# Optimization experiments

Hardware: AMD Instinct MI355X
Metric: run time of the kernel (lower is better)

The kernel has to match this reference:

```python
import jax, jax.numpy as jnp
import numpy as np

WINDOW = (1, 7, 7)
DIM_HEAD = 32


def _rel_pos_index(ws):
    d, h, w = ws
    coords = np.stack(np.meshgrid(np.arange(d), np.arange(h), np.arange(w), indexing='ij'))
    cf = coords.reshape(3, -1)                      # [3, N]
    rel = (cf[:, :, None] - cf[:, None, :]).transpose(1, 2, 0).copy()  # [N, N, 3]
    rel[..., 0] += d - 1
    rel[..., 1] += h - 1
    rel[..., 2] += w - 1
    rel[..., 0] *= (2 * h - 1) * (2 * w - 1)
    rel[..., 1] *= (2 * w - 1)
    return jnp.asarray(rel.sum(-1))                 # [N, N] int32, N = 49


REL_IDX = _rel_pos_index(WINDOW)


def setup_inputs() -> dict:
    key = jax.random.key(0)
    k1, k2, k3, k4, k5 = jax.random.split(key, 5)
    B, X, Y, W1, W2, D = 4, 32, 32, 7, 7, 512
    heads = D // DIM_HEAD
    n_bias = (2 * WINDOW[0] - 1) * (2 * WINDOW[1] - 1) * (2 * WINDOW[2] - 1)  # 169
    s = 1.0 / np.sqrt(D)
    return {
        'x': jax.random.normal(k1, (B, X, Y, W1, W2, D), jnp.float32),
        'y': jax.random.normal(k2, (B, X, Y, W1, W2, D), jnp.float32),
        'Wq': jax.random.normal(k3, (D, D), jnp.float32) * s,
        'Wkv': jax.random.normal(k4, (D, 2 * D), jnp.float32) * s,
        'bias_table': jax.random.normal(k5, (n_bias, heads), jnp.float32) * 0.02,
    }


def reference(x, y, Wq, Wkv, bias_table):
    B, X, Y, W1, W2, D = x.shape
    h = D // DIM_HEAD
    n = W1 * W2                                     # 49 tokens per window
    scale = DIM_HEAD ** -0.5

    xr = x.reshape(B * X * Y, n, D)                 # [Bw, n, D]
    yr = y.reshape(B * X * Y, n, D)

    q = xr @ Wq                                     # [Bw, n, D]
    kv = yr @ Wkv                                   # [Bw, n, 2D]
    k, v = kv[..., :D], kv[..., D:]

    def to_heads(t):
        return t.reshape(t.shape[0], n, h, DIM_HEAD).transpose(0, 2, 1, 3)  # [Bw, h, n, dh]

    q, k, v = to_heads(q), to_heads(k), to_heads(v)

    sim = jnp.einsum('bhid,bhjd->bhij', q, k) * scale   # [Bw, h, n, n]
    bias = bias_table[REL_IDX]                          # [n, n, h]
    sim = sim + bias.transpose(2, 0, 1)[None]           # broadcast over windows

    attn = jax.nn.softmax(sim, axis=-1)
    out = jnp.einsum('bhij,bhjd->bhid', attn, v)        # [Bw, h, n, dh]
    out = out.transpose(0, 2, 1, 3).reshape(B * X * Y, W1, W2, D)
    return out.reshape(B, X, Y, W1, W2, D)
```

## Files before the change

kernel.cpp:

```cpp
#include <hip/hip_runtime.h>


typedef __bf16 bf16x8 __attribute__((ext_vector_type(8)));
typedef __attribute__((ext_vector_type(4))) float f32x4;

#define DEVI __device__ __forceinline__

DEVI unsigned short f2bf(float f) {
  union { float f; unsigned u; } v; v.f = f;
  unsigned r = v.u + 0x7FFFu + ((v.u >> 16) & 1u);
  return (unsigned short)(r >> 16);
}

#define MFMA16(a, b, c) __builtin_amdgcn_mfma_f32_16x16x32_bf16((a), (b), (c), 0, 0, 0)

__global__ void prep_kernel(const float* __restrict__ Wq, const float* __restrict__ Wkv,
                            const float* __restrict__ bt, char* __restrict__ ws) {
  int t = blockIdx.x * 256 + threadIdx.x;
  if (t < 786432) {
    int e = t & 7, lane = (t >> 3) & 63, ks = (t >> 9) & 15, nt = (t >> 13) & 1,
        h = (t >> 14) & 15, T = t >> 18;
    int row = ks * 32 + (lane >> 4) * 8 + e;
    int col = h * 32 + nt * 16 + (lane & 15);
    float v;
    if (T == 0)      v = Wq[row * 512 + col] * 0.17677669529663687f;
    else if (T == 1) v = Wkv[row * 1024 + col];
    else             v = Wkv[row * 1024 + 512 + col];
    ((unsigned short*)ws)[t] = f2bf(v);
  }
  if (t < 262144) {
    int r = t & 3, lane = (t >> 2) & 63, nt = (t >> 8) & 3, mt = (t >> 10) & 3,
        h = (t >> 12) & 15;
    int i = mt * 16 + (lane >> 4) * 4 + r;
    int j = nt * 16 + (lane & 15);
    float v;
    if (j >= 49)      v = -1e30f;
    else if (i >= 49) v = 0.0f;
    else {
      int hi = i / 7, wi = i % 7, hj = j / 7, wj = j % 7;
      v = bt[((hi - hj + 6) * 13 + (wi - wj + 6)) * 16 + h];
    }
    ((float*)(ws + 1572864))[t] = v;
  }
}

DEVI bf16x8 ldXY(const char* base, int row, int kc) {
  unsigned a = ((unsigned)(row * 1024 + kc * 2)) ^ (((unsigned)row & 7u) << 4);
  return *(const bf16x8*)(base + a);
}
DEVI bf16x8 ldXY_c(const char* base, int row, int kc) {
  int rc = row < 48 ? row : 48;
  bf16x8 v = ldXY(base, rc, kc);
  if (row > 48) {
    union { long long z[2]; bf16x8 v; } u; u.z[0] = 0; u.z[1] = 0;
    v = u.v;
  }
  return v;
}
DEVI bf16x8 ldQK(const char* base, int row, int kc) {
  int rc = row < 48 ? row : 48;
  unsigned a = ((unsigned)(rc * 64 + kc * 2)) ^ (((unsigned)rc & 3u) << 4);
  return *(const bf16x8*)(base + a);
}
DEVI bf16x8 ldP(const char* base, int row, int kc) {
  int rc = row < 48 ? row : 48;
  unsigned a = ((unsigned)(rc * 128 + kc * 2)) ^ (((unsigned)rc & 7u) << 4);
  return *(const bf16x8*)(base + a);
}
DEVI bf16x8 ldVT(const char* base, int dh, int kc) {
  unsigned a = ((unsigned)(dh * 128 + kc * 2)) ^ (((unsigned)dh & 7u) << 4);
  return *(const bf16x8*)(base + a);
}

__global__ __launch_bounds__(512, 2)
void attn_kernel(const float* __restrict__ x, const float* __restrict__ y,
                 const char* __restrict__ wsW, const float* __restrict__ biasD,
                 float* __restrict__ out) {
  extern __shared__ char smem[];
  char* xb = smem;
  char* yb = smem + 50176;
  const int tid = threadIdx.x;
  const int lane = tid & 63, wave = tid >> 6;
  const int p = wave >> 1, sub = wave & 1;
  const int g = lane >> 4, lr = lane & 15;
  char* wb = smem + 100352 + p * 10624;
  char* qb = wb;
  char* kb = wb + 3136;
  char* vt = wb + 6272;
  char* pb = wb;
  float* sb = (float*)(wb + 10368);

  const int bw = blockIdx.x;
  const float* xs = x + (size_t)bw * 25088;
  const float* ys = y + (size_t)bw * 25088;

  for (int it = tid; it < 6272; it += 512) {
    float4 v = ((const float4*)xs)[it];
    float4 w = ((const float4*)ys)[it];
    int i = it >> 7;
    int k = (it & 127) << 2;
    unsigned a = ((unsigned)(i * 1024 + k * 2)) ^ (((unsigned)i & 7u) << 4);
    uint2 ux, uy;
    ux.x = (unsigned)f2bf(v.x) | ((unsigned)f2bf(v.y) << 16);
    ux.y = (unsigned)f2bf(v.z) | ((unsigned)f2bf(v.w) << 16);
    uy.x = (unsigned)f2bf(w.x) | ((unsigned)f2bf(w.y) << 16);
    uy.y = (unsigned)f2bf(w.z) | ((unsigned)f2bf(w.w) << 16);
    *(uint2*)(xb + a) = ux;
    *(uint2*)(yb + a) = uy;
  }

  const bf16x8* wsQ = (const bf16x8*)wsW;
  const bf16x8* wsK = (const bf16x8*)(wsW + 524288);
  const bf16x8* wsV = (const bf16x8*)(wsW + 1048576);
  const f32x4* bD = (const f32x4*)biasD;
  const f32x4 fz = {0.f, 0.f, 0.f, 0.f};

  for (int hi = 0; hi < 4; ++hi) {
    const int h = p * 4 + hi;

    __syncthreads();

    f32x4 accq[4];
    #pragma unroll
    for (int mt = 0; mt < 4; ++mt) accq[mt] = fz;
    {
      const bf16x8* pQ = wsQ + (size_t)((h * 2 + sub) * 16) * 64 + lane;
      bf16x8 bq[16];
      #pragma unroll
      for (int ks = 0; ks < 16; ++ks) bq[ks] = pQ[ks * 64];
      #pragma unroll
      for (int ks = 0; ks < 16; ++ks) {
        int kc = ks * 32 + g * 8;
        accq[0] = MFMA16(ldXY(xb, lr, kc),        bq[ks], accq[0]);
        accq[1] = MFMA16(ldXY(xb, lr + 16, kc),   bq[ks], accq[1]);
        accq[2] = MFMA16(ldXY(xb, lr + 32, kc),   bq[ks], accq[2]);
        accq[3] = MFMA16(ldXY_c(xb, lr + 48, kc), bq[ks], accq[3]);
      }
    }
    #pragma unroll
    for (int mt = 0; mt < 4; ++mt)
      #pragma unroll
      for (int r = 0; r < 4; ++r) {
        int row = mt * 16 + g * 4 + r;
        if (row < 49) {
          unsigned a = ((unsigned)(row * 64 + (sub * 16 + lr) * 2)) ^ (((unsigned)row & 3u) << 4);
          *(unsigned short*)(qb + a) = f2bf(accq[mt][r]);
        }
      }

    f32x4 acck[4], accv[4];
    #pragma unroll
    for (int mt = 0; mt < 4; ++mt) { acck[mt] = fz; accv[mt] = fz; }
    {
      const bf16x8* pK = wsK + (size_t)((h * 2 + sub) * 16) * 64 + lane;
      const bf16x8* pV = wsV + (size_t)((h * 2 + sub) * 16) * 64 + lane;
      bf16x8 ksr[8], vsr[8];
      #pragma unroll
      for (int i = 0; i < 8; ++i) { ksr[i] = pK[i * 64]; vsr[i] = pV[i * 64]; }
      #pragma unroll
      for (int ks = 0; ks < 16; ++ks) {
        bf16x8 bk = ksr[ks & 7], bv = vsr[ks & 7];
        if (ks < 8) {
          ksr[ks & 7] = pK[(ks + 8) * 64];
          vsr[ks & 7] = pV[(ks + 8) * 64];
        }
        int kc = ks * 32 + g * 8;
        bf16x8 a0 = ldXY(yb, lr, kc);
        bf16x8 a1 = ldXY(yb, lr + 16, kc);
        bf16x8 a2 = ldXY(yb, lr + 32, kc);
        bf16x8 a3 = ldXY_c(yb, lr + 48, kc);
        acck[0] = MFMA16(a0, bk, acck[0]);
        acck[1] = MFMA16(a1, bk, acck[1]);
        acck[2] = MFMA16(a2, bk, acck[2]);
        acck[3] = MFMA16(a3, bk, acck[3]);
        accv[0] = MFMA16(a0, bv, accv[0]);
        accv[1] = MFMA16(a1, bv, accv[1]);
        accv[2] = MFMA16(a2, bv, accv[2]);
        accv[3] = MFMA16(a3, bv, accv[3]);
      }
    }
    #pragma unroll
    for (int mt = 0; mt < 4; ++mt) {
      #pragma unroll
      for (int r = 0; r < 4; ++r) {
        int row = mt * 16 + g * 4 + r;
        if (row < 49) {
          unsigned a = ((unsigned)(row * 64 + (sub * 16 + lr) * 2)) ^ (((unsigned)row & 3u) << 4);
          *(unsigned short*)(kb + a) = f2bf(acck[mt][r]);
        }
      }
      int dh = sub * 16 + lr;
      int t0 = mt * 16 + g * 4;
      unsigned av = ((unsigned)(dh * 128 + t0 * 2)) ^ (((unsigned)dh & 7u) << 4);
      uint2 pk;
      pk.x = (unsigned)f2bf(accv[mt][0]) | ((unsigned)f2bf(accv[mt][1]) << 16);
      pk.y = (unsigned)f2bf(accv[mt][2]) | ((unsigned)f2bf(accv[mt][3]) << 16);
      *(uint2*)(vt + av) = pk;
    }

    __syncthreads();

    f32x4 bias[2][4];
    #pragma unroll
    for (int mi = 0; mi < 2; ++mi)
      #pragma unroll
      for (int nt = 0; nt < 4; ++nt)
        bias[mi][nt] = bD[(size_t)(((h * 4 + sub * 2 + mi) * 4 + nt) * 64 + lane)];

    bf16x8 qa[2], kf[4];
    #pragma unroll
    for (int mi = 0; mi < 2; ++mi) qa[mi] = ldQK(qb, sub * 32 + mi * 16 + lr, g * 8);
    #pragma unroll
    for (int nt = 0; nt < 4; ++nt) kf[nt] = ldQK(kb, nt * 16 + lr, g * 8);
    f32x4 accs[2][4];
    #pragma unroll
    for (int mi = 0; mi < 2; ++mi)
      #pragma unroll
      for (int nt = 0; nt < 4; ++nt)
        accs[mi][nt] = MFMA16(qa[mi], kf[nt], fz);

    float sinv[2][4];
    #pragma unroll
    for (int mi = 0; mi < 2; ++mi) {
      f32x4 vals[4];
      #pragma unroll
      for (int nt = 0; nt < 4; ++nt)
        vals[nt] = accs[mi][nt] + bias[mi][nt];
      #pragma unroll
      for (int r = 0; r < 4; ++r) {
        float m = fmaxf(fmaxf(vals[0][r], vals[1][r]), fmaxf(vals[2][r], vals[3][r]));
        m = fmaxf(m, __shfl_xor(m, 1));
        m = fmaxf(m, __shfl_xor(m, 2));
        m = fmaxf(m, __shfl_xor(m, 4));
        m = fmaxf(m, __shfl_xor(m, 8));
        float s = 0.f;
        #pragma unroll
        for (int nt = 0; nt < 4; ++nt) {
          float pv = __expf(vals[nt][r] - m);
          vals[nt][r] = pv;
          s += pv;
        }
        s += __shfl_xor(s, 1);
        s += __shfl_xor(s, 2);
        s += __shfl_xor(s, 4);
        s += __shfl_xor(s, 8);
        sinv[mi][r] = 1.0f / s;
      }
      accs[mi][0] = vals[0]; accs[mi][1] = vals[1];
      accs[mi][2] = vals[2]; accs[mi][3] = vals[3];
    }

    __syncthreads();

    #pragma unroll
    for (int mi = 0; mi < 2; ++mi) {
      int mt_g = sub * 2 + mi;
      #pragma unroll
      for (int r = 0; r < 4; ++r) {
        int row = mt_g * 16 + g * 4 + r;
        if (row < 49) {
          #pragma unroll
          for (int nt = 0; nt < 4; ++nt) {
            unsigned a = ((unsigned)(row * 128 + (nt * 16 + lr) * 2)) ^ (((unsigned)row & 7u) << 4);
            *(unsigned short*)(pb + a) = f2bf(accs[mi][nt][r]);
          }
          if (lr == 0) sb[row] = sinv[mi][r];
        }
      }
    }

    f32x4 acco[2][2];
    acco[0][0] = fz; acco[0][1] = fz; acco[1][0] = fz; acco[1][1] = fz;
    #pragma unroll
    for (int ks = 0; ks < 2; ++ks) {
      int jc = ks * 32 + g * 8;
      bf16x8 av0 = ldVT(vt, lr, jc);
      bf16x8 av1 = ldVT(vt, lr + 16, jc);
      bf16x8 bp0 = ldP(pb, (sub * 2 + 0) * 16 + lr, jc);
      bf16x8 bp1 = ldP(pb, (sub * 2 + 1) * 16 + lr, jc);
      acco[0][0] = MFMA16(av0, bp0, acco[0][0]);
      acco[0][1] = MFMA16(av0, bp1, acco[0][1]);
      acco[1][0] = MFMA16(av1, bp0, acco[1][0]);
      acco[1][1] = MFMA16(av1, bp1, acco[1][1]);
    }

    float* ow = out + (size_t)bw * 25088 + h * 32;
    #pragma unroll
    for (int ntl = 0; ntl < 2; ++ntl) {
      int tok = (sub * 2 + ntl) * 16 + lr;
      if (tok < 49) {
        float inv = sb[tok];
        #pragma unroll
        for (int mt = 0; mt < 2; ++mt) {
          f32x4 vv = acco[mt][ntl];
          vv[0] *= inv; vv[1] *= inv; vv[2] *= inv; vv[3] *= inv;
          *(f32x4*)(&ow[(size_t)tok * 512 + mt * 16 + g * 4]) = vv;
        }
      }
    }
  }
}

extern "C" void kernel_launch(void* const* d_in, const int* in_sizes, int n_in,
                              void* d_out, int out_size, void* d_ws, size_t ws_size,
                              hipStream_t stream) {
  (void)in_sizes; (void)n_in; (void)out_size; (void)ws_size;
  const float* x = (const float*)d_in[0];
  const float* y = (const float*)d_in[1];
  const float* Wq = (const float*)d_in[2];
  const float* Wkv = (const float*)d_in[3];
  const float* bt = (const float*)d_in[4];
  float* out = (float*)d_out;
  char* ws = (char*)d_ws;

  prep_kernel<<<3072, 256, 0, stream>>>(Wq, Wkv, bt, ws);

  (void)hipFuncSetAttribute((const void*)attn_kernel,
                            hipFuncAttributeMaxDynamicSharedMemorySize, 142848);
  attn_kernel<<<4096, 512, 142848, stream>>>(x, y, (const char*)ws,
                                             (const float*)(ws + 1572864), out);
}
```

Measured before the change: 792.6 us.

## Transpose score MFMA for lane-local softmax, fold normalization, pair Q projections

Result: slower. 843.2 us (+6.4%).

```diff
diff --git a/kernel.cpp b/kernel.cpp
--- a/kernel.cpp
+++ b/kernel.cpp
@@ -11,8 +11,16 @@
   unsigned r = v.u + 0x7FFFu + ((v.u >> 16) & 1u);
   return (unsigned short)(r >> 16);
 }
+DEVI unsigned pkbf(float a, float b) {
+  return (unsigned)f2bf(a) | ((unsigned)f2bf(b) << 16);
+}
 
 #define MFMA16(a, b, c) __builtin_amdgcn_mfma_f32_16x16x32_bf16((a), (b), (c), 0, 0, 0)
+
+#define SWZ_Y(r)  ((((unsigned)(r)) & 7u) << 4)
+#define SWZ_A(r)  (((((unsigned)(r)) >> 2) & 3u) << 5)
+#define SWZ_P(r)  ((((unsigned)(r)) & 7u) << 4)
+#define SWZ_VT(r) ((((unsigned)(r)) & 7u) << 4)
 
 __global__ void prep_kernel(const float* __restrict__ Wq, const float* __restrict__ Wkv,
                             const float* __restrict__ bt, char* __restrict__ ws) {
@@ -31,8 +39,8 @@
   if (t < 262144) {
     int r = t & 3, lane = (t >> 2) & 63, nt = (t >> 8) & 3, mt = (t >> 10) & 3,
         h = (t >> 12) & 15;
-    int i = mt * 16 + (lane >> 4) * 4 + r;
-    int j = nt * 16 + (lane & 15);
+    int i = mt * 16 + (lane & 15);
+    int j = nt * 16 + ((lane >> 4) & 3) * 4 + r;
     float v;
     if (j >= 49)      v = -1e30f;
     else if (i >= 49) v = 0.0f;
@@ -45,7 +53,7 @@
 }
 
 DEVI bf16x8 ldXY(const char* base, int row, int kc) {
-  unsigned a = ((unsigned)(row * 1024 + kc * 2)) ^ (((unsigned)row & 7u) << 4);
+  unsigned a = ((unsigned)(row * 1024 + kc * 2)) ^ SWZ_Y(row);
   return *(const bf16x8*)(base + a);
 }
 DEVI bf16x8 ldXY_c(const char* base, int row, int kc) {
@@ -57,18 +65,18 @@
   }
   return v;
 }
-DEVI bf16x8 ldQK(const char* base, int row, int kc) {
+DEVI bf16x8 ldA(const char* base, int row, int kc) {
   int rc = row < 48 ? row : 48;
-  unsigned a = ((unsigned)(rc * 64 + kc * 2)) ^ (((unsigned)rc & 3u) << 4);
+  unsigned a = ((unsigned)(rc * 64 + kc * 2)) ^ SWZ_A(rc);
   return *(const bf16x8*)(base + a);
 }
-DEVI bf16x8 ldP(const char* base, int row, int kc) {
+DEVI bf16x8 ldP2(const char* base, int row, int jc) {
   int rc = row < 48 ? row : 48;
-  unsigned a = ((unsigned)(rc * 128 + kc * 2)) ^ (((unsigned)rc & 7u) << 4);
+  unsigned a = ((unsigned)(rc * 128 + jc * 2)) ^ SWZ_P(rc);
   return *(const bf16x8*)(base + a);
 }
-DEVI bf16x8 ldVT(const char* base, int dh, int kc) {
-  unsigned a = ((unsigned)(dh * 128 + kc * 2)) ^ (((unsigned)dh & 7u) << 4);
+DEVI bf16x8 ldVT(const char* base, int dh, int jc) {
+  unsigned a = ((unsigned)(dh * 128 + jc * 2)) ^ SWZ_VT(dh);
   return *(const bf16x8*)(base + a);
 }
 
@@ -83,12 +91,11 @@
   const int lane = tid & 63, wave = tid >> 6;
   const int p = wave >> 1, sub = wave & 1;
   const int g = lane >> 4, lr = lane & 15;
-  char* wb = smem + 100352 + p * 10624;
-  char* qb = wb;
-  char* kb = wb + 3136;
-  char* vt = wb + 6272;
-  char* pb = wb;
-  float* sb = (float*)(wb + 10368);
+  char* pbase = smem + 100352 + p * 15872;
+  char* qAb = pbase;
+  char* kbuf = pbase + 3136;
+  char* qBb = pbase + 6272;
+  char* vt = pbase + 9408;
 
   const int bw = blockIdx.x;
   const float* xs = x + (size_t)bw * 25088;
@@ -99,12 +106,10 @@
     float4 w = ((const float4*)ys)[it];
     int i = it >> 7;
     int k = (it & 127) << 2;
-    unsigned a = ((unsigned)(i * 1024 + k * 2)) ^ (((unsigned)i & 7u) << 4);
+    unsigned a = ((unsigned)(i * 1024 + k * 2)) ^ SWZ_Y(i);
     uint2 ux, uy;
-    ux.x = (unsigned)f2bf(v.x) | ((unsigned)f2bf(v.y) << 16);
-    ux.y = (unsigned)f2bf(v.z) | ((unsigned)f2bf(v.w) << 16);
-    uy.x = (unsigned)f2bf(w.x) | ((unsigned)f2bf(w.y) << 16);
-    uy.y = (unsigned)f2bf(w.z) | ((unsigned)f2bf(w.w) << 16);
+    ux.x = pkbf(v.x, v.y); ux.y = pkbf(v.z, v.w);
+    uy.x = pkbf(w.x, w.y); uy.y = pkbf(w.z, w.w);
     *(uint2*)(xb + a) = ux;
     *(uint2*)(yb + a) = uy;
   }
@@ -115,91 +120,62 @@
   const f32x4* bD = (const f32x4*)biasD;
   const f32x4 fz = {0.f, 0.f, 0.f, 0.f};
 
-  for (int hi = 0; hi < 4; ++hi) {
-    const int h = p * 4 + hi;
-
-    __syncthreads();
-
-    f32x4 accq[4];
-    #pragma unroll
-    for (int mt = 0; mt < 4; ++mt) accq[mt] = fz;
-    {
-      const bf16x8* pQ = wsQ + (size_t)((h * 2 + sub) * 16) * 64 + lane;
-      bf16x8 bq[16];
-      #pragma unroll
-      for (int ks = 0; ks < 16; ++ks) bq[ks] = pQ[ks * 64];
-      #pragma unroll
-      for (int ks = 0; ks < 16; ++ks) {
-        int kc = ks * 32 + g * 8;
-        accq[0] = MFMA16(ldXY(xb, lr, kc),        bq[ks], accq[0]);
-        accq[1] = MFMA16(ldXY(xb, lr + 16, kc),   bq[ks], accq[1]);
-        accq[2] = MFMA16(ldXY(xb, lr + 32, kc),   bq[ks], accq[2]);
-        accq[3] = MFMA16(ldXY_c(xb, lr + 48, kc), bq[ks], accq[3]);
-      }
-    }
+  auto storeQK = [&](char* qb, f32x4 (&acc)[4]) {
     #pragma unroll
     for (int mt = 0; mt < 4; ++mt)
       #pragma unroll
       for (int r = 0; r < 4; ++r) {
         int row = mt * 16 + g * 4 + r;
         if (row < 49) {
-          unsigned a = ((unsigned)(row * 64 + (sub * 16 + lr) * 2)) ^ (((unsigned)row & 3u) << 4);
-          *(unsigned short*)(qb + a) = f2bf(accq[mt][r]);
+          unsigned a = ((unsigned)(row * 64 + (sub * 16 + lr) * 2)) ^ SWZ_A(row);
+          *(unsigned short*)(qb + a) = f2bf(acc[mt][r]);
         }
       }
-
-    f32x4 acck[4], accv[4];
-    #pragma unroll
-    for (int mt = 0; mt < 4; ++mt) { acck[mt] = fz; accv[mt] = fz; }
-    {
-      const bf16x8* pK = wsK + (size_t)((h * 2 + sub) * 16) * 64 + lane;
-      const bf16x8* pV = wsV + (size_t)((h * 2 + sub) * 16) * 64 + lane;
-      bf16x8 ksr[8], vsr[8];
-      #pragma unroll
-      for (int i = 0; i < 8; ++i) { ksr[i] = pK[i * 64]; vsr[i] = pV[i * 64]; }
-      #pragma unroll
-      for (int ks = 0; ks < 16; ++ks) {
-        bf16x8 bk = ksr[ks & 7], bv = vsr[ks & 7];
-        if (ks < 8) {
-          ksr[ks & 7] = pK[(ks + 8) * 64];
-          vsr[ks & 7] = pV[(ks + 8) * 64];
-        }
-        int kc = ks * 32 + g * 8;
-        bf16x8 a0 = ldXY(yb, lr, kc);
-        bf16x8 a1 = ldXY(yb, lr + 16, kc);
-        bf16x8 a2 = ldXY(yb, lr + 32, kc);
-        bf16x8 a3 = ldXY_c(yb, lr + 48, kc);
-        acck[0] = MFMA16(a0, bk, acck[0]);
-        acck[1] = MFMA16(a1, bk, acck[1]);
-        acck[2] = MFMA16(a2, bk, acck[2]);
-        acck[3] = MFMA16(a3, bk, acck[3]);
-        accv[0] = MFMA16(a0, bv, accv[0]);
-        accv[1] = MFMA16(a1, bv, accv[1]);
-        accv[2] = MFMA16(a2, bv, accv[2]);
-        accv[3] = MFMA16(a3, bv, accv[3]);
-      }
-    }
+  };
+
+  auto kv_compute = [&](int h, f32x4 (&ak)[4], f32x4 (&av)[4]) {
+    #pragma unroll
+    for (int mt = 0; mt < 4; ++mt) { ak[mt] = fz; av[mt] = fz; }
+    const bf16x8* pK = wsK + (size_t)((h * 2 + sub) * 16) * 64 + lane;
+    const bf16x8* pV = wsV + (size_t)((h * 2 + sub) * 16) * 64 + lane;
+    bf16x8 ksr[8], vsr[8];
+    #pragma unroll
+    for (int i = 0; i < 8; ++i) { ksr[i] = pK[i * 64]; vsr[i] = pV[i * 64]; }
+    #pragma unroll
+    for (int ks = 0; ks < 16; ++ks) {
+      bf16x8 bk = ksr[ks & 7], bv = vsr[ks & 7];
+      if (ks < 8) { ksr[ks & 7] = pK[(ks + 8) * 64]; vsr[ks & 7] = pV[(ks + 8) * 64]; }
+      int kc = ks * 32 + g * 8;
+      bf16x8 a0 = ldXY(yb, lr, kc);
+      bf16x8 a1 = ldXY(yb, lr + 16, kc);
+      bf16x8 a2 = ldXY(yb, lr + 32, kc);
+      bf16x8 a3 = ldXY_c(yb, lr + 48, kc);
+      ak[0] = MFMA16(a0, bk, ak[0]);
+      ak[1] = MFMA16(a1, bk, ak[1]);
+      ak[2] = MFMA16(a2, bk, ak[2]);
+      ak[3] = MFMA16(a3, bk, ak[3]);
+      av[0] = MFMA16(a0, bv, av[0]);
+      av[1] = MFMA16(a1, bv, av[1]);
+      av[2] = MFMA16(a2, bv, av[2]);
+      av[3] = MFMA16(a3, bv, av[3]);
+    }
+  };
+
+  auto kv_store = [&](f32x4 (&ak)[4], f32x4 (&av)[4]) {
+    storeQK(kbuf, ak);
     #pragma unroll
     for (int mt = 0; mt < 4; ++mt) {
-      #pragma unroll
-      for (int r = 0; r < 4; ++r) {
-        int row = mt * 16 + g * 4 + r;
-        if (row < 49) {
-          unsigned a = ((unsigned)(row * 64 + (sub * 16 + lr) * 2)) ^ (((unsigned)row & 3u) << 4);
-          *(unsigned short*)(kb + a) = f2bf(acck[mt][r]);
-        }
-      }
       int dh = sub * 16 + lr;
       int t0 = mt * 16 + g * 4;
-      unsigned av = ((unsigned)(dh * 128 + t0 * 2)) ^ (((unsigned)dh & 7u) << 4);
+      unsigned a = ((unsigned)(dh * 128 + t0 * 2)) ^ SWZ_VT(dh);
       uint2 pk;
-      pk.x = (unsigned)f2bf(accv[mt][0]) | ((unsigned)f2bf(accv[mt][1]) << 16);
-      pk.y = (unsigned)f2bf(accv[mt][2]) | ((unsigned)f2bf(accv[mt][3]) << 16);
-      *(uint2*)(vt + av) = pk;
-    }
-
-    __syncthreads();
-
+      pk.x = pkbf(av[mt][0], av[mt][1]);
+      pk.y = pkbf(av[mt][2], av[mt][3]);
+      *(uint2*)(vt + a) = pk;
+    }
+  };
+
+  auto attn_head = [&](int h, const char* qbuf, char* Pb) {
     f32x4 bias[2][4];
     #pragma unroll
     for (int mi = 0; mi < 2; ++mi)
@@ -209,62 +185,59 @@
 
     bf16x8 qa[2], kf[4];
     #pragma unroll
-    for (int mi = 0; mi < 2; ++mi) qa[mi] = ldQK(qb, sub * 32 + mi * 16 + lr, g * 8);
-    #pragma unroll
-    for (int nt = 0; nt < 4; ++nt) kf[nt] = ldQK(kb, nt * 16 + lr, g * 8);
+    for (int mi = 0; mi < 2; ++mi) qa[mi] = ldA(qbuf, sub * 32 + mi * 16 + lr, g * 8);
+    #pragma unroll
+    for (int nt = 0; nt < 4; ++nt) kf[nt] = ldA(kbuf, nt * 16 + lr, g * 8);
+
     f32x4 accs[2][4];
     #pragma unroll
     for (int mi = 0; mi < 2; ++mi)
       #pragma unroll
       for (int nt = 0; nt < 4; ++nt)
-        accs[mi][nt] = MFMA16(qa[mi], kf[nt], fz);
-
-    float sinv[2][4];
+        accs[mi][nt] = MFMA16(kf[nt], qa[mi], fz);
+
+    uint2 pks[2][4];
     #pragma unroll
     for (int mi = 0; mi < 2; ++mi) {
       f32x4 vals[4];
       #pragma unroll
+      for (int nt = 0; nt < 4; ++nt) vals[nt] = accs[mi][nt] + bias[mi][nt];
+      float m = vals[0][0];
+      #pragma unroll
       for (int nt = 0; nt < 4; ++nt)
-        vals[nt] = accs[mi][nt] + bias[mi][nt];
-      #pragma unroll
-      for (int r = 0; r < 4; ++r) {
-        float m = fmaxf(fmaxf(vals[0][r], vals[1][r]), fmaxf(vals[2][r], vals[3][r]));
-        m = fmaxf(m, __shfl_xor(m, 1));
-        m = fmaxf(m, __shfl_xor(m, 2));
-        m = fmaxf(m, __shfl_xor(m, 4));
-        m = fmaxf(m, __shfl_xor(m, 8));
-        float s = 0.f;
         #pragma unroll
-        for (int nt = 0; nt < 4; ++nt) {
+        for (int r = 0; r < 4; ++r) m = fmaxf(m, vals[nt][r]);
+      m = fmaxf(m, __shfl_xor(m, 16));
+      m = fmaxf(m, __shfl_xor(m, 32));
+      float s = 0.f;
+      #pragma unroll
+      for (int nt = 0; nt < 4; ++nt)
+        #pragma unroll
+        for (int r = 0; r < 4; ++r) {
           float pv = __expf(vals[nt][r] - m);
           vals[nt][r] = pv;
           s += pv;
         }
-        s += __shfl_xor(s, 1);
-        s += __shfl_xor(s, 2);
-        s += __shfl_xor(s, 4);
-        s += __shfl_xor(s, 8);
-        sinv[mi][r] = 1.0f / s;
-      }
-      accs[mi][0] = vals[0]; accs[mi][1] = vals[1];
-      accs[mi][2] = vals[2]; accs[mi][3] = vals[3];
+      s += __shfl_xor(s, 16);
+      s += __shfl_xor(s, 32);
+      float inv = 1.0f / s;
+      #pragma unroll
+      for (int nt = 0; nt < 4; ++nt) {
+        pks[mi][nt].x = pkbf(vals[nt][0] * inv, vals[nt][1] * inv);
+        pks[mi][nt].y = pkbf(vals[nt][2] * inv, vals[nt][3] * inv);
+      }
     }
 
     __syncthreads();
 
     #pragma unroll
     for (int mi = 0; mi < 2; ++mi) {
-      int mt_g = sub * 2 + mi;
-      #pragma unroll
-      for (int r = 0; r < 4; ++r) {
-        int row = mt_g * 16 + g * 4 + r;
-        if (row < 49) {
-          #pragma unroll
-          for (int nt = 0; nt < 4; ++nt) {
-            unsigned a = ((unsigned)(row * 128 + (nt * 16 + lr) * 2)) ^ (((unsigned)row & 7u) << 4);
-            *(unsigned short*)(pb + a) = f2bf(accs[mi][nt][r]);
-          }
-          if (lr == 0) sb[row] = sinv[mi][r];
+      int i = sub * 32 + mi * 16 + lr;
+      if (i < 49) {
+        #pragma unroll
+        for (int nt = 0; nt < 4; ++nt) {
+          unsigned a = ((unsigned)(i * 128 + (nt * 16 + g * 4) * 2)) ^ SWZ_P(i);
+          *(uint2*)(Pb + a) = pks[mi][nt];
         }
       }
     }
@@ -276,8 +249,8 @@
       int jc = ks * 32 + g * 8;
       bf16x8 av0 = ldVT(vt, lr, jc);
       bf16x8 av1 = ldVT(vt, lr + 16, jc);
-      bf16x8 bp0 = ldP(pb, (sub * 2 + 0) * 16 + lr, jc);
-      bf16x8 bp1 = ldP(pb, (sub * 2 + 1) * 16 + lr, jc);
+      bf16x8 bp0 = ldP2(Pb, sub * 32 + lr, jc);
+      bf16x8 bp1 = ldP2(Pb, sub * 32 + 16 + lr, jc);
       acco[0][0] = MFMA16(av0, bp0, acco[0][0]);
       acco[0][1] = MFMA16(av0, bp1, acco[0][1]);
       acco[1][0] = MFMA16(av1, bp0, acco[1][0]);
@@ -286,18 +259,72 @@
 
     float* ow = out + (size_t)bw * 25088 + h * 32;
     #pragma unroll
-    for (int ntl = 0; ntl < 2; ++ntl) {
-      int tok = (sub * 2 + ntl) * 16 + lr;
+    for (int it = 0; it < 2; ++it) {
+      int tok = sub * 32 + it * 16 + lr;
       if (tok < 49) {
-        float inv = sb[tok];
         #pragma unroll
-        for (int mt = 0; mt < 2; ++mt) {
-          f32x4 vv = acco[mt][ntl];
-          vv[0] *= inv; vv[1] *= inv; vv[2] *= inv; vv[3] *= inv;
-          *(f32x4*)(&ow[(size_t)tok * 512 + mt * 16 + g * 4]) = vv;
-        }
-      }
-    }
+        for (int dt = 0; dt < 2; ++dt)
+          *(f32x4*)(&ow[(size_t)tok * 512 + dt * 16 + g * 4]) = acco[dt][it];
+      }
+    }
+  };
+
+  for (int hp = 0; hp < 2; ++hp) {
+    const int hA = p * 4 + hp * 2, hB = hA + 1;
+
+    __syncthreads();
+
+    f32x4 aqA[4], aqB[4];
+    #pragma unroll
+    for (int mt = 0; mt < 4; ++mt) { aqA[mt] = fz; aqB[mt] = fz; }
+    {
+      const bf16x8* pQA = wsQ + (size_t)((hA * 2 + sub) * 16) * 64 + lane;
+      const bf16x8* pQB = wsQ + (size_t)((hB * 2 + sub) * 16) * 64 + lane;
+      bf16x8 ra[8], rb[8];
+      #pragma unroll
+      for (int i = 0; i < 8; ++i) { ra[i] = pQA[i * 64]; rb[i] = pQB[i * 64]; }
+      #pragma unroll
+      for (int ks = 0; ks < 16; ++ks) {
+        bf16x8 fa = ra[ks & 7], fb = rb[ks & 7];
+        if (ks < 8) { ra[ks & 7] = pQA[(ks + 8) * 64]; rb[ks & 7] = pQB[(ks + 8) * 64]; }
+        int kc = ks * 32 + g * 8;
+        bf16x8 a0 = ldXY(xb, lr, kc);
+        bf16x8 a1 = ldXY(xb, lr + 16, kc);
+        bf16x8 a2 = ldXY(xb, lr + 32, kc);
+        bf16x8 a3 = ldXY_c(xb, lr + 48, kc);
+        aqA[0] = MFMA16(a0, fa, aqA[0]);
+        aqA[1] = MFMA16(a1, fa, aqA[1]);
+        aqA[2] = MFMA16(a2, fa, aqA[2]);
+        aqA[3] = MFMA16(a3, fa, aqA[3]);
+        aqB[0] = MFMA16(a0, fb, aqB[0]);
+        aqB[1] = MFMA16(a1, fb, aqB[1]);
+        aqB[2] = MFMA16(a2, fb, aqB[2]);
+        aqB[3] = MFMA16(a3, fb, aqB[3]);
+      }
+    }
+    storeQK(qAb, aqA);
+    storeQK(qBb, aqB);
+
+    {
+      f32x4 ak[4], av[4];
+      kv_compute(hA, ak, av);
+      kv_store(ak, av);
+    }
+
+    __syncthreads();
+
+    attn_head(hA, qAb, pbase);
+
+    {
+      f32x4 ak[4], av[4];
+      kv_compute(hB, ak, av);
+      __syncthreads();
+      kv_store(ak, av);
+    }
+
+    __syncthreads();
+
+    attn_head(hB, qBb, pbase + 3136);
   }
 }
 
@@ -316,7 +343,7 @@
   prep_kernel<<<3072, 256, 0, stream>>>(Wq, Wkv, bt, ws);
 
   (void)hipFuncSetAttribute((const void*)attn_kernel,
-                            hipFuncAttributeMaxDynamicSharedMemorySize, 142848);
-  attn_kernel<<<4096, 512, 142848, stream>>>(x, y, (const char*)ws,
+                            hipFuncAttributeMaxDynamicSharedMemorySize, 163840);
+  attn_kernel<<<4096, 512, 163840, stream>>>(x, y, (const char*)ws,
                                              (const float*)(ws + 1572864), out);
 }
```

## Project two heads per pass to reuse X/Y LDS fragments

Applied to the files above, without the earlier changes.

Measured after the change: 1.207 ms. +52.3%, slower.

```diff
diff --git a/kernel.cpp b/kernel.cpp
--- a/kernel.cpp
+++ b/kernel.cpp
@@ -10,6 +10,12 @@
   union { float f; unsigned u; } v; v.f = f;
   unsigned r = v.u + 0x7FFFu + ((v.u >> 16) & 1u);
   return (unsigned short)(r >> 16);
+}
+DEVI unsigned pkbf(float a, float b) {
+  return (unsigned)f2bf(a) | ((unsigned)f2bf(b) << 16);
+}
+DEVI uint2 pk4(const f32x4& a) {
+  uint2 r; r.x = pkbf(a[0], a[1]); r.y = pkbf(a[2], a[3]); return r;
 }
 
 #define MFMA16(a, b, c) __builtin_amdgcn_mfma_f32_16x16x32_bf16((a), (b), (c), 0, 0, 0)
@@ -83,12 +89,13 @@
   const int lane = tid & 63, wave = tid >> 6;
   const int p = wave >> 1, sub = wave & 1;
   const int g = lane >> 4, lr = lane & 15;
-  char* wb = smem + 100352 + p * 10624;
-  char* qb = wb;
-  char* kb = wb + 3136;
-  char* vt = wb + 6272;
-  char* pb = wb;
-  float* sb = (float*)(wb + 10368);
+  char* pbase = smem + 100352 + p * 14720;
+  char* qb = pbase;
+  char* kb = pbase + 3136;
+  char* vtA = pbase + 6272;
+  char* vtB = pbase + 10368;
+  char* pb = pbase;
+  float* sb = (float*)(pbase + 14464);
 
   const int bw = blockIdx.x;
   const float* xs = x + (size_t)bw * 25088;
@@ -101,10 +108,8 @@
     int k = (it & 127) << 2;
     unsigned a = ((unsigned)(i * 1024 + k * 2)) ^ (((unsigned)i & 7u) << 4);
     uint2 ux, uy;
-    ux.x = (unsigned)f2bf(v.x) | ((unsigned)f2bf(v.y) << 16);
-    ux.y = (unsigned)f2bf(v.z) | ((unsigned)f2bf(v.w) << 16);
-    uy.x = (unsigned)f2bf(w.x) | ((unsigned)f2bf(w.y) << 16);
-    uy.y = (unsigned)f2bf(w.z) | ((unsigned)f2bf(w.w) << 16);
+    ux.x = pkbf(v.x, v.y); ux.y = pkbf(v.z, v.w);
+    uy.x = pkbf(w.x, w.y); uy.y = pkbf(w.z, w.w);
     *(uint2*)(xb + a) = ux;
     *(uint2*)(yb + a) = uy;
   }
@@ -115,28 +120,7 @@
   const f32x4* bD = (const f32x4*)biasD;
   const f32x4 fz = {0.f, 0.f, 0.f, 0.f};
 
-  for (int hi = 0; hi < 4; ++hi) {
-    const int h = p * 4 + hi;
-
-    __syncthreads();
-
-    f32x4 accq[4];
-    #pragma unroll
-    for (int mt = 0; mt < 4; ++mt) accq[mt] = fz;
-    {
-      const bf16x8* pQ = wsQ + (size_t)((h * 2 + sub) * 16) * 64 + lane;
-      bf16x8 bq[16];
-      #pragma unroll
-      for (int ks = 0; ks < 16; ++ks) bq[ks] = pQ[ks * 64];
-      #pragma unroll
-      for (int ks = 0; ks < 16; ++ks) {
-        int kc = ks * 32 + g * 8;
-        accq[0] = MFMA16(ldXY(xb, lr, kc),        bq[ks], accq[0]);
-        accq[1] = MFMA16(ldXY(xb, lr + 16, kc),   bq[ks], accq[1]);
-        accq[2] = MFMA16(ldXY(xb, lr + 32, kc),   bq[ks], accq[2]);
-        accq[3] = MFMA16(ldXY_c(xb, lr + 48, kc), bq[ks], accq[3]);
-      }
-    }
+  auto storeQK = [&](char* dst, f32x4 (&acc)[4]) {
     #pragma unroll
     for (int mt = 0; mt < 4; ++mt)
       #pragma unroll
@@ -144,62 +128,47 @@
         int row = mt * 16 + g * 4 + r;
         if (row < 49) {
           unsigned a = ((unsigned)(row * 64 + (sub * 16 + lr) * 2)) ^ (((unsigned)row & 3u) << 4);
-          *(unsigned short*)(qb + a) = f2bf(accq[mt][r]);
-        }
-      }
-
-    f32x4 acck[4], accv[4];
-    #pragma unroll
-    for (int mt = 0; mt < 4; ++mt) { acck[mt] = fz; accv[mt] = fz; }
-    {
-      const bf16x8* pK = wsK + (size_t)((h * 2 + sub) * 16) * 64 + lane;
-      const bf16x8* pV = wsV + (size_t)((h * 2 + sub) * 16) * 64 + lane;
-      bf16x8 ksr[8], vsr[8];
-      #pragma unroll
-      for (int i = 0; i < 8; ++i) { ksr[i] = pK[i * 64]; vsr[i] = pV[i * 64]; }
-      #pragma unroll
-      for (int ks = 0; ks < 16; ++ks) {
-        bf16x8 bk = ksr[ks & 7], bv = vsr[ks & 7];
-        if (ks < 8) {
-          ksr[ks & 7] = pK[(ks + 8) * 64];
-          vsr[ks & 7] = pV[(ks + 8) * 64];
-        }
-        int kc = ks * 32 + g * 8;
-        bf16x8 a0 = ldXY(yb, lr, kc);
-        bf16x8 a1 = ldXY(yb, lr + 16, kc);
-        bf16x8 a2 = ldXY(yb, lr + 32, kc);
-        bf16x8 a3 = ldXY_c(yb, lr + 48, kc);
-        acck[0] = MFMA16(a0, bk, acck[0]);
-        acck[1] = MFMA16(a1, bk, acck[1]);
-        acck[2] = MFMA16(a2, bk, acck[2]);
-        acck[3] = MFMA16(a3, bk, acck[3]);
-        accv[0] = MFMA16(a0, bv, accv[0]);
-        accv[1] = MFMA16(a1, bv, accv[1]);
-        accv[2] = MFMA16(a2, bv, accv[2]);
-        accv[3] = MFMA16(a3, bv, accv[3]);
-      }
-    }
+          *(unsigned short*)(dst + a) = f2bf(acc[mt][r]);
+        }
+      }
+  };
+  auto storeQKp = [&](char* dst, uint2 (&pk)[4]) {
     #pragma unroll
     for (int mt = 0; mt < 4; ++mt) {
+      int row0 = mt * 16 + g * 4;
+      unsigned colb = (unsigned)((sub * 16 + lr) * 2);
+      unsigned u[4] = { pk[mt].x & 0xFFFFu, pk[mt].x >> 16,
+                        pk[mt].y & 0xFFFFu, pk[mt].y >> 16 };
       #pragma unroll
       for (int r = 0; r < 4; ++r) {
-        int row = mt * 16 + g * 4 + r;
+        int row = row0 + r;
         if (row < 49) {
-          unsigned a = ((unsigned)(row * 64 + (sub * 16 + lr) * 2)) ^ (((unsigned)row & 3u) << 4);
-          *(unsigned short*)(kb + a) = f2bf(acck[mt][r]);
-        }
-      }
+          unsigned a = ((unsigned)(row * 64) + colb) ^ (((unsigned)row & 3u) << 4);
+          *(unsigned short*)(dst + a) = (unsigned short)u[r];
+        }
+      }
+    }
+  };
+  auto storeVT = [&](char* vt, f32x4 (&acc)[4]) {
+    #pragma unroll
+    for (int mt = 0; mt < 4; ++mt) {
       int dh = sub * 16 + lr;
       int t0 = mt * 16 + g * 4;
-      unsigned av = ((unsigned)(dh * 128 + t0 * 2)) ^ (((unsigned)dh & 7u) << 4);
-      uint2 pk;
-      pk.x = (unsigned)f2bf(accv[mt][0]) | ((unsigned)f2bf(accv[mt][1]) << 16);
-      pk.y = (unsigned)f2bf(accv[mt][2]) | ((unsigned)f2bf(accv[mt][3]) << 16);
-      *(uint2*)(vt + av) = pk;
-    }
-
-    __syncthreads();
-
+      unsigned a = ((unsigned)(dh * 128 + t0 * 2)) ^ (((unsigned)dh & 7u) << 4);
+      *(uint2*)(vt + a) = pk4(acc[mt]);
+    }
+  };
+  auto storeVTp = [&](char* vt, uint2 (&pk)[4]) {
+    #pragma unroll
+    for (int mt = 0; mt < 4; ++mt) {
+      int dh = sub * 16 + lr;
+      int t0 = mt * 16 + g * 4;
+      unsigned a = ((unsigned)(dh * 128 + t0 * 2)) ^ (((unsigned)dh & 7u) << 4);
+      *(uint2*)(vt + a) = pk[mt];
+    }
+  };
+
+  auto attn_head = [&](int h, const char* vt) {
     f32x4 bias[2][4];
     #pragma unroll
     for (int mi = 0; mi < 2; ++mi)
@@ -224,8 +193,7 @@
     for (int mi = 0; mi < 2; ++mi) {
       f32x4 vals[4];
       #pragma unroll
-      for (int nt = 0; nt < 4; ++nt)
-        vals[nt] = accs[mi][nt] + bias[mi][nt];
+      for (int nt = 0; nt < 4; ++nt) vals[nt] = accs[mi][nt] + bias[mi][nt];
       #pragma unroll
       for (int r = 0; r < 4; ++r) {
         float m = fmaxf(fmaxf(vals[0][r], vals[1][r]), fmaxf(vals[2][r], vals[3][r]));
@@ -298,6 +266,112 @@
         }
       }
     }
+  };
+
+  for (int hp = 0; hp < 2; ++hp) {
+    const int hA = p * 4 + hp * 2, hB = hA + 1;
+
+    __syncthreads();
+
+    f32x4 aqA[4], aqB[4];
+    #pragma unroll
+    for (int mt = 0; mt < 4; ++mt) { aqA[mt] = fz; aqB[mt] = fz; }
+    {
+      const bf16x8* pQA = wsQ + (size_t)((hA * 2 + sub) * 16) * 64 + lane;
+      const bf16x8* pQB = wsQ + (size_t)((hB * 2 + sub) * 16) * 64 + lane;
+      bf16x8 ra[8], rb[8];
+      #pragma unroll
+      for (int i = 0; i < 8; ++i) { ra[i] = pQA[i * 64]; rb[i] = pQB[i * 64]; }
+      #pragma unroll
+      for (int ks = 0; ks < 16; ++ks) {
+        bf16x8 fa = ra[ks & 7], fb = rb[ks & 7];
+        if (ks < 8) { ra[ks & 7] = pQA[(ks + 8) * 64]; rb[ks & 7] = pQB[(ks + 8) * 64]; }
+        int kc = ks * 32 + g * 8;
+        bf16x8 a0 = ldXY(xb, lr, kc);
+        bf16x8 a1 = ldXY(xb, lr + 16, kc);
+        bf16x8 a2 = ldXY(xb, lr + 32, kc);
+        bf16x8 a3 = ldXY_c(xb, lr + 48, kc);
+        aqA[0] = MFMA16(a0, fa, aqA[0]);
+        aqA[1] = MFMA16(a1, fa, aqA[1]);
+        aqA[2] = MFMA16(a2, fa, aqA[2]);
+        aqA[3] = MFMA16(a3, fa, aqA[3]);
+        aqB[0] = MFMA16(a0, fb, aqB[0]);
+        aqB[1] = MFMA16(a1, fb, aqB[1]);
+        aqB[2] = MFMA16(a2, fb, aqB[2]);
+        aqB[3] = MFMA16(a3, fb, aqB[3]);
+      }
+    }
+    storeQK(qb, aqA);
+    uint2 qBp[4];
+    #pragma unroll
+    for (int mt = 0; mt < 4; ++mt) qBp[mt] = pk4(aqB[mt]);
+
+    f32x4 akA[4], avA[4], akB[4], avB[4];
+    #pragma unroll
+    for (int mt = 0; mt < 4; ++mt) {
+      akA[mt] = fz; avA[mt] = fz; akB[mt] = fz; avB[mt] = fz;
+    }
+    {
+      const bf16x8* pKA = wsK + (size_t)((hA * 2 + sub) * 16) * 64 + lane;
+      const bf16x8* pKB = wsK + (size_t)((hB * 2 + sub) * 16) * 64 + lane;
+      const bf16x8* pVA = wsV + (size_t)((hA * 2 + sub) * 16) * 64 + lane;
+      const bf16x8* pVB = wsV + (size_t)((hB * 2 + sub) * 16) * 64 + lane;
+      bf16x8 rkA[4], rkB[4], rvA[4], rvB[4];
+      #pragma unroll
+      for (int i = 0; i < 4; ++i) {
+        rkA[i] = pKA[i * 64]; rkB[i] = pKB[i * 64];
+        rvA[i] = pVA[i * 64]; rvB[i] = pVB[i * 64];
+      }
+      #pragma unroll
+      for (int ks = 0; ks < 16; ++ks) {
+        bf16x8 bkA = rkA[ks & 3], bkB = rkB[ks & 3];
+        bf16x8 bvA = rvA[ks & 3], bvB = rvB[ks & 3];
+        if (ks < 12) {
+          rkA[ks & 3] = pKA[(ks + 4) * 64]; rkB[ks & 3] = pKB[(ks + 4) * 64];
+          rvA[ks & 3] = pVA[(ks + 4) * 64]; rvB[ks & 3] = pVB[(ks + 4) * 64];
+        }
+        int kc = ks * 32 + g * 8;
+        bf16x8 a0 = ldXY(yb, lr, kc);
+        bf16x8 a1 = ldXY(yb, lr + 16, kc);
+        bf16x8 a2 = ldXY(yb, lr + 32, kc);
+        bf16x8 a3 = ldXY_c(yb, lr + 48, kc);
+        akA[0] = MFMA16(a0, bkA, akA[0]);
+        akA[1] = MFMA16(a1, bkA, akA[1]);
+        akA[2] = MFMA16(a2, bkA, akA[2]);
+        akA[3] = MFMA16(a3, bkA, akA[3]);
+        avA[0] = MFMA16(a0, bvA, avA[0]);
+        avA[1] = MFMA16(a1, bvA, avA[1]);
+        avA[2] = MFMA16(a2, bvA, avA[2]);
+        avA[3] = MFMA16(a3, bvA, avA[3]);
+        akB[0] = MFMA16(a0, bkB, akB[0]);
+        akB[1] = MFMA16(a1, bkB, akB[1]);
+        akB[2] = MFMA16(a2, bkB, akB[2]);
+        akB[3] = MFMA16(a3, bkB, akB[3]);
+        avB[0] = MFMA16(a0, bvB, avB[0]);
+        avB[1] = MFMA16(a1, bvB, avB[1]);
+        avB[2] = MFMA16(a2, bvB, avB[2]);
+        avB[3] = MFMA16(a3, bvB, avB[3]);
+      }
+    }
+    storeQK(kb, akA);
+    storeVT(vtA, avA);
+    uint2 kBp[4], vBp[4];
+    #pragma unroll
+    for (int mt = 0; mt < 4; ++mt) { kBp[mt] = pk4(akB[mt]); vBp[mt] = pk4(avB[mt]); }
+
+    __syncthreads();
+
+    attn_head(hA, vtA);
+
+    __syncthreads();
+
+    storeQKp(qb, qBp);
+    storeQKp(kb, kBp);
+    storeVTp(vtB, vBp);
+
+    __syncthreads();
+
+    attn_head(hB, vtB);
   }
 }
 
@@ -316,7 +390,7 @@
   prep_kernel<<<3072, 256, 0, stream>>>(Wq, Wkv, bt, ws);
 
   (void)hipFuncSetAttribute((const void*)attn_kernel,
-                            hipFuncAttributeMaxDynamicSharedMemorySize, 142848);
-  attn_kernel<<<4096, 512, 142848, stream>>>(x, y, (const char*)ws,
+                            hipFuncAttributeMaxDynamicSharedMemorySize, 159232);
+  attn_kernel<<<4096, 512, 159232, stream>>>(x, y, (const char*)ws,
                                              (const float*)(ws + 1572864), out);
 }
```
